# Performance work log

Hardware: AMD Instinct MI355X
Metric: run time of the kernel (lower is better)

The kernel has to match this reference:

```python
import jax, jax.numpy as jnp
import numpy as np

B, N, K, D, H, PQ, PV = 2, 2048, 30, 128, 4, 8, 4
INV3C = float(np.sqrt(1.0 / (3 * D)))      # 1/sqrt(3*hidden_dim)
INV3 = float(np.sqrt(1.0 / 3.0))
PT_SCALE = float(np.sqrt(1.0 / (3 * (PQ * 9.0 / 2))))


def _gather(nodes, idx):
    # nodes [B,N,...], idx [B,N,K] -> [B,N,K,...]
    return jax.vmap(lambda n, i: n[i])(nodes, idx)


def _ln(x, w, b, eps=1e-5):
    mu = x.mean(-1, keepdims=True)
    var = x.var(-1, keepdims=True)
    return (x - mu) / jnp.sqrt(var + eps) * w + b


def _forward(h_V, h_E, E_idx, R, t, mask_attend, mask_V,
             Wq, bq, Wkv, bkv, Wqp, bqp, Wkvp, bkvp, Wb, bb_, head_weights,
             Wout, bout, ln0_w, ln0_b, ln1_w, ln1_b, Wm1, bm1, Wm2, bm2):
    q = (h_V @ Wq + bq).reshape(B, N, H, D)                     # [B,N,H,C]
    kv = (h_V @ Wkv + bkv).reshape(B, N, H, 2 * D)
    k_, v_ = kv[..., :D], kv[..., D:]

    def apply_rigid(pts):  # pts [B,N,P,3] -> R @ p + t
        return jnp.einsum('bnxy,bnpy->bnpx', R, pts) + t[:, :, None, :]

    # torch builds points by split-into-3-then-stack along last dim
    qp = h_V @ Wqp + bqp                                        # [B,N,H*PQ*3]
    q_pts = jnp.stack(jnp.split(qp, 3, axis=-1), axis=-1)       # [B,N,H*PQ,3]
    q_pts = apply_rigid(q_pts).reshape(B, N, H, PQ, 3)
    kvp = h_V @ Wkvp + bkvp
    kv_pts = jnp.stack(jnp.split(kvp, 3, axis=-1), axis=-1)
    kv_pts = apply_rigid(kv_pts).reshape(B, N, H, PQ + PV, 3)
    k_pts, v_pts = kv_pts[..., :PQ, :], kv_pts[..., PQ:, :]

    b_bias = h_E @ Wb + bb_                                     # [B,N,K,H]
    k_nb = _gather(k_, E_idx)                                   # [B,N,K,H,C]
    a = jnp.einsum('bnhc,bnkhc->bnkh', q, k_nb) * INV3C
    a = a + INV3 * b_bias

    kp_nb = _gather(k_pts, E_idx)                               # [B,N,K,H,PQ,3]
    diff = q_pts[:, :, None] - kp_nb
    pt_att = jnp.sum(diff * diff, axis=-1)                      # [B,N,K,H,PQ]
    hw = jax.nn.softplus(head_weights)                          # [H]
    pt_att = jnp.sum(PT_SCALE * hw[None, None, None, :, None] * pt_att, axis=-1) * -0.5

    att_mask = 100000.0 * (mask_attend - 1.0)                   # [B,N,K]
    a = a + pt_att + att_mask[..., None]
    a = jax.nn.softmax(a, axis=-2)                              # softmax over neighbors K

    v_nb = _gather(v_, E_idx)
    o = jnp.einsum('bnkh,bnkhc->bnhc', a, v_nb).reshape(B, N, H * D)
    vp_nb = _gather(v_pts, E_idx)                               # [B,N,K,H,PV,3]
    o_pt = jnp.einsum('bnkh,bnkhpx->bnhpx', a, vp_nb)
    # invert_apply: R^T (x - t)
    o_pt = jnp.einsum('bnyx,bnhpy->bnhpx', R, o_pt - t[:, :, None, None, :])
    o_pt_norm = jnp.sqrt(jnp.sum(o_pt ** 2, axis=-1) + 1e-8).reshape(B, N, H * PV)
    o_pt = o_pt.reshape(B, N, H * PV, 3)
    o_pair = jnp.einsum('bnkh,bnkc->bnhc', a, h_E).reshape(B, N, H * D)

    cat = jnp.concatenate([o, o_pt[..., 0], o_pt[..., 1], o_pt[..., 2], o_pt_norm, o_pair], axis=-1)
    s = cat @ Wout + bout

    hv = _ln(h_V + s, ln0_w, ln0_b)
    m = jax.nn.relu(hv @ Wm1 + bm1) @ Wm2 + bm2
    hv = _ln(hv + m, ln1_w, ln1_b)
    return hv * mask_V[..., None]


def setup_inputs() -> dict:
    key = jax.random.key(0)
    ks = jax.random.split(key, 16)

    def dense(k, fi, fo):
        kw, kb = jax.random.split(k)
        s = 1.0 / np.sqrt(fi)
        return (jax.random.uniform(kw, (fi, fo), jnp.float32, -s, s),
                jax.random.uniform(kb, (fo,), jnp.float32, -s, s))

    h_V = jax.random.normal(ks[0], (B, N, D), jnp.float32)
    h_E = jax.random.normal(ks[1], (B, N, K, D), jnp.float32)
    E_idx = jax.random.randint(ks[2], (B, N, K), 0, N)
    Rr = jax.random.normal(ks[3], (B, N, 3, 3), jnp.float32)
    R, _ = jnp.linalg.qr(Rr)  # proper orthonormal frames
    t = jax.random.normal(ks[4], (B, N, 3), jnp.float32)
    mask_attend = jnp.ones((B, N, K), jnp.float32)
    mask_V = jnp.ones((B, N), jnp.float32)

    Wq, bq = dense(ks[5], D, D * H)
    Wkv, bkv = dense(ks[6], D, 2 * D * H)
    Wqp, bqp = dense(ks[7], D, H * PQ * 3)
    Wkvp, bkvp = dense(ks[8], D, H * (PQ + PV) * 3)
    Wb, bb_ = dense(ks[9], D, H)
    head_weights = jnp.full((H,), 0.541324854612918, jnp.float32)
    out_dim = H * (D + D + 4 * PV)
    Wout, bout = dense(ks[10], out_dim, D)
    ln0_w = jnp.ones((D,), jnp.float32); ln0_b = jnp.zeros((D,), jnp.float32)
    ln1_w = jnp.ones((D,), jnp.float32); ln1_b = jnp.zeros((D,), jnp.float32)
    Wm1, bm1 = dense(ks[11], D, 4 * D)
    Wm2, bm2 = dense(ks[12], 4 * D, D)
    return dict(h_V=h_V, h_E=h_E, E_idx=E_idx, R=R, t=t,
                mask_attend=mask_attend, mask_V=mask_V,
                Wq=Wq, bq=bq, Wkv=Wkv, bkv=bkv, Wqp=Wqp, bqp=bqp,
                Wkvp=Wkvp, bkvp=bkvp, Wb=Wb, bb_=bb_, head_weights=head_weights,
                Wout=Wout, bout=bout, ln0_w=ln0_w, ln0_b=ln0_b,
                ln1_w=ln1_w, ln1_b=ln1_b, Wm1=Wm1, bm1=bm1, Wm2=Wm2, bm2=bm2)


def reference(h_V, h_E, E_idx, R, t, mask_attend, mask_V,
              Wq, bq, Wkv, bkv, Wqp, bqp, Wkvp, bkvp, Wb, bb_, head_weights,
              Wout, bout, ln0_w, ln0_b, ln1_w, ln1_b, Wm1, bm1, Wm2, bm2):
    return _forward(h_V, h_E, E_idx, R, t, mask_attend, mask_V,
                    Wq, bq, Wkv, bkv, Wqp, bqp, Wkvp, bkvp, Wb, bb_, head_weights,
                    Wout, bout, ln0_w, ln0_b, ln1_w, ln1_b, Wm1, bm1, Wm2, bm2)
```

## Files before the change

kernel.cpp:

```cpp
#include <hip/hip_runtime.h>
#include <math.h>

#define BB 2
#define NN 2048
#define KK 30
#define DD 128
#define HH 4
#define PQ_ 8
#define PV_ 4
#define NPB 8
#define TM 16

#define INV3C    0.05103103630798288f
#define INV3     0.5773502691896258f
#define PT_SCALE 0.09622504486493764f

typedef __attribute__((ext_vector_type(8))) short short8;
typedef __attribute__((ext_vector_type(4))) float f32x4;
typedef __attribute__((ext_vector_type(4))) unsigned short us4;
typedef unsigned short ushort_t;

__device__ __forceinline__ ushort_t f2bf(float f) {
    unsigned u = __float_as_uint(f);
    unsigned r = u + 0x7FFFu + ((u >> 16) & 1u);
    return (ushort_t)(r >> 16);
}
__device__ __forceinline__ float bf2f(ushort_t u) {
    return __uint_as_float(((unsigned)u) << 16);
}

__device__ __forceinline__ void fma4(float4& a, float s, const float4& w) {
    a.x = fmaf(s, w.x, a.x);
    a.y = fmaf(s, w.y, a.y);
    a.z = fmaf(s, w.z, a.z);
    a.w = fmaf(s, w.w, a.w);
}

__global__ __launch_bounds__(256) void prep_kernel(
    const float* __restrict__ Wout, const float* __restrict__ Wm1,
    const float* __restrict__ Wm2,
    ushort_t* __restrict__ WoutT, ushort_t* __restrict__ Wm1T,
    ushort_t* __restrict__ Wm2T)
{
    const int stride = gridDim.x * blockDim.x;
    const int t0 = blockIdx.x * blockDim.x + threadIdx.x;
    for (int idx = t0; idx < 128 * 1088; idx += stride) {
        int n = idx / 1088, k = idx - n * 1088;
        WoutT[idx] = f2bf(Wout[(size_t)k * 128 + n]);
    }
    for (int idx = t0; idx < 512 * 128; idx += stride) {
        int n = idx >> 7, k = idx & 127;
        Wm1T[idx] = f2bf(Wm1[(size_t)k * 512 + n]);
    }
    for (int idx = t0; idx < 128 * 512; idx += stride) {
        int n = idx >> 9, k = idx & 511;
        Wm2T[idx] = f2bf(Wm2[(size_t)k * 128 + n]);
    }
}

__global__ __launch_bounds__(256, 4) void proj_kernel(
    const float* __restrict__ hV, const float* __restrict__ R, const float* __restrict__ tvec,
    const float* __restrict__ Wq, const float* __restrict__ bq,
    const float* __restrict__ Wkv, const float* __restrict__ bkv,
    const float* __restrict__ Wqp, const float* __restrict__ bqp,
    const float* __restrict__ Wkvp, const float* __restrict__ bkvp,
    float* __restrict__ q, ushort_t* __restrict__ kb, ushort_t* __restrict__ vb,
    float* __restrict__ qpts, float* __restrict__ kpts, float* __restrict__ vpts)
{
    const int node0 = (blockIdx.x >> 1) * NPB;
    const int half  = blockIdx.x & 1;
    const int tid = threadIdx.x;
    __shared__ float4 sx4[NPB][32];
    __shared__ float4 sqp4[NPB][24];
    __shared__ float4 skvp4[NPB][36];

    {
        const float4* src = (const float4*)(hV + (size_t)node0 * DD);
        sx4[tid >> 5][tid & 31] = src[tid];
    }
    __syncthreads();

    if (tid < 222) {
        const int Q = half * 222 + tid;
        const float* W; const float* bias; int ncols, col, dest;
        if (Q < 128)      { W = Wq;   bias = bq;   ncols = 512;  col = Q * 4;         dest = 0; }
        else if (Q < 384) { W = Wkv;  bias = bkv;  ncols = 1024; col = (Q - 128) * 4; dest = 1; }
        else if (Q < 408) { W = Wqp;  bias = bqp;  ncols = 96;   col = (Q - 384) * 4; dest = 2; }
        else              { W = Wkvp; bias = bkvp; ncols = 144;  col = (Q - 408) * 4; dest = 3; }

        float4 acc[NPB];
        #pragma unroll
        for (int r = 0; r < NPB; ++r) acc[r] = make_float4(0.f, 0.f, 0.f, 0.f);

        float4 w0 = *(const float4*)&W[(size_t)0 * ncols + col];
        float4 w1 = *(const float4*)&W[(size_t)1 * ncols + col];
        float4 w2 = *(const float4*)&W[(size_t)2 * ncols + col];
        float4 w3 = *(const float4*)&W[(size_t)3 * ncols + col];
        for (int i = 0; i < DD; i += 4) {
            float4 n0, n1, n2, n3;
            if (i + 4 < DD) {
                n0 = *(const float4*)&W[(size_t)(i + 4) * ncols + col];
                n1 = *(const float4*)&W[(size_t)(i + 5) * ncols + col];
                n2 = *(const float4*)&W[(size_t)(i + 6) * ncols + col];
                n3 = *(const float4*)&W[(size_t)(i + 7) * ncols + col];
            }
            #pragma unroll
            for (int r = 0; r < NPB; ++r) {
                float4 x = sx4[r][i >> 2];
                fma4(acc[r], x.x, w0);
                fma4(acc[r], x.y, w1);
                fma4(acc[r], x.z, w2);
                fma4(acc[r], x.w, w3);
            }
            w0 = n0; w1 = n1; w2 = n2; w3 = n3;
        }

        float4 bv = *(const float4*)&bias[col];
        if (dest == 0) {
            #pragma unroll
            for (int r = 0; r < NPB; ++r) {
                float4 o = make_float4(acc[r].x + bv.x, acc[r].y + bv.y,
                                       acc[r].z + bv.z, acc[r].w + bv.w);
                *(float4*)&q[(size_t)(node0 + r) * 512 + col] = o;
            }
        } else if (dest == 1) {
            int h = col >> 8, wcol = col & 255;
            ushort_t* base = (wcol < 128) ? kb : vb;
            int off = h * DD + (wcol & 127);
            #pragma unroll
            for (int r = 0; r < NPB; ++r) {
                us4 o;
                o.x = f2bf(acc[r].x + bv.x);
                o.y = f2bf(acc[r].y + bv.y);
                o.z = f2bf(acc[r].z + bv.z);
                o.w = f2bf(acc[r].w + bv.w);
                *(us4*)&base[(size_t)(node0 + r) * 512 + off] = o;
            }
        } else if (dest == 2) {
            #pragma unroll
            for (int r = 0; r < NPB; ++r) {
                float4 o = make_float4(acc[r].x + bv.x, acc[r].y + bv.y,
                                       acc[r].z + bv.z, acc[r].w + bv.w);
                sqp4[r][col >> 2] = o;
            }
        } else {
            #pragma unroll
            for (int r = 0; r < NPB; ++r) {
                float4 o = make_float4(acc[r].x + bv.x, acc[r].y + bv.y,
                                       acc[r].z + bv.z, acc[r].w + bv.w);
                skvp4[r][col >> 2] = o;
            }
        }
    }
    __syncthreads();

    if (half == 1) {
        const float* sqp_s  = (const float*)&sqp4[0][0];
        const float* skvp_s = (const float*)&skvp4[0][0];

        for (int idx = tid; idx < NPB * 96; idx += 256) {
            int r = idx / 96, u = idx % 96;
            int j = u / 3, d = u % 3;
            int node = node0 + r;
            float acc = tvec[node * 3 + d];
            #pragma unroll
            for (int y = 0; y < 3; ++y)
                acc = fmaf(R[node * 9 + d * 3 + y], sqp_s[r * 96 + y * 32 + j], acc);
            qpts[(size_t)node * 96 + j * 3 + d] = acc;
        }
        for (int idx = tid; idx < NPB * 144; idx += 256) {
            int r = idx / 144, u = idx % 144;
            int jj = u / 3, d = u % 3;
            int node = node0 + r;
            float acc = tvec[node * 3 + d];
            #pragma unroll
            for (int y = 0; y < 3; ++y)
                acc = fmaf(R[node * 9 + d * 3 + y], skvp_s[r * 144 + y * 48 + jj], acc);
            int hh = jj / 12, pp = jj % 12;
            if (pp < PQ_) kpts[(size_t)node * 96 + (hh * PQ_ + pp) * 3 + d] = acc;
            else          vpts[(size_t)node * 48 + (hh * PV_ + (pp - PQ_)) * 3 + d] = acc;
        }
    }
}

__global__ __launch_bounds__(256, 8) void attn_kernel(
    const float* __restrict__ hE, const int* __restrict__ Eidx,
    const float* __restrict__ R, const float* __restrict__ tvec,
    const float* __restrict__ mask_att,
    const float* __restrict__ Wb, const float* __restrict__ bb,
    const float* __restrict__ head_w,
    const float* __restrict__ q, const ushort_t* __restrict__ kb,
    const ushort_t* __restrict__ vb,
    const float* __restrict__ qpts, const float* __restrict__ kpts, const float* __restrict__ vpts,
    ushort_t* __restrict__ catb)
{
    const int node = blockIdx.x;
    const int b = node >> 11;
    const int tid = threadIdx.x;
    const int lane = tid & 63;
    const int wv = tid >> 6;

    __shared__ ushort_t s_hEb[KK * DD];
    __shared__ float s_cat[1088];
    __shared__ float s_qp[96];
    __shared__ float s_p[HH][32];
    __shared__ int   s_j[32];
    __shared__ float s_mask[32];
    __shared__ float s_opt[48];

    if (tid < 96) s_qp[tid] = qpts[(size_t)node * 96 + tid];
    if (tid < KK) {
        s_j[tid] = Eidx[(size_t)node * KK + tid];
        s_mask[tid] = 100000.0f * (mask_att[(size_t)node * KK + tid] - 1.0f);
    }
    __syncthreads();

    const int h = wv;
    const int l32 = lane & 31;
    const int g = lane >> 5;
    const float* hE_node = hE + (size_t)node * (KK * DD);

    const float q0  = q[(size_t)node * 512 + h * DD + l32];
    const float q1  = q[(size_t)node * 512 + h * DD + l32 + 32];
    const float q2  = q[(size_t)node * 512 + h * DD + l32 + 64];
    const float q3  = q[(size_t)node * 512 + h * DD + l32 + 96];
    const float wb0 = Wb[(l32 +  0) * HH + h];
    const float wb1 = Wb[(l32 + 32) * HH + h];
    const float wb2 = Wb[(l32 + 64) * HH + h];
    const float wb3 = Wb[(l32 + 96) * HH + h];
    const float cpt = -0.5f * PT_SCALE * log1pf(expf(head_w[h]));
    const float bbh = INV3 * bb[h];
    const float qpl = (l32 < 24) ? s_qp[h * 24 + l32] : 0.f;

    for (int kx2 = 0; kx2 < KK / 2; ++kx2) {
        const int k = kx2 * 2 + g;
        size_t jb = (size_t)(b * NN + s_j[k]);
        const ushort_t* kr = kb + jb * 512 + h * DD;
        float k0 = bf2f(kr[l32]),      k1 = bf2f(kr[l32 + 32]);
        float k2 = bf2f(kr[l32 + 64]), k3 = bf2f(kr[l32 + 96]);
        float s = q0 * k0 + q1 * k1 + q2 * k2 + q3 * k3;
        const float* her = hE_node + k * DD;
        float h0 = her[l32], h1 = her[l32 + 32], h2 = her[l32 + 64], h3 = her[l32 + 96];
        if (wv == 0) {
            s_hEb[k * DD + l32]      = f2bf(h0);
            s_hEb[k * DD + l32 + 32] = f2bf(h1);
            s_hEb[k * DD + l32 + 64] = f2bf(h2);
            s_hEb[k * DD + l32 + 96] = f2bf(h3);
        }
        float t = wb0 * h0 + wb1 * h1 + wb2 * h2 + wb3 * h3;
        float ptc = 0.f;
        if (l32 < 24) {
            float d = qpl - kpts[jb * 96 + h * 24 + l32];
            ptc = d * d;
        }
        float val = INV3C * s + INV3 * t + cpt * ptc;
        #pragma unroll
        for (int off = 16; off; off >>= 1) val += __shfl_down(val, off, 32);
        if (l32 == 0) s_p[h][k] = val + bbh + s_mask[k];
    }
    __syncthreads();

    {
        float v = (lane < KK) ? s_p[h][lane] : -INFINITY;
        float m = v;
        #pragma unroll
        for (int off = 16; off; off >>= 1) m = fmaxf(m, __shfl_down(m, off));
        m = __shfl(m, 0);
        float e = (lane < KK) ? expf(v - m) : 0.f;
        float s = e;
        #pragma unroll
        for (int off = 16; off; off >>= 1) s += __shfl_down(s, off);
        s = __shfl(s, 0);
        if (lane < KK) s_p[h][lane] = e / s;
    }
    __syncthreads();

    {
        const int oh = tid >> 6;
        const int oc0 = (tid & 63) * 2;
        float a0 = 0.f, a1 = 0.f;
        for (int kx = 0; kx < KK; ++kx) {
            size_t jb = (size_t)(b * NN + s_j[kx]);
            unsigned pv = *(const unsigned*)&vb[jb * 512 + oh * DD + oc0];
            float p = s_p[oh][kx];
            a0 = fmaf(p, bf2f((ushort_t)(pv & 0xffff)), a0);
            a1 = fmaf(p, bf2f((ushort_t)(pv >> 16)), a1);
        }
        s_cat[oh * DD + oc0]     = a0;
        s_cat[oh * DD + oc0 + 1] = a1;
        float b0 = 0.f, b1 = 0.f;
        for (int kx = 0; kx < KK; ++kx) {
            unsigned pe = *(const unsigned*)&s_hEb[kx * DD + oc0];
            float p = s_p[oh][kx];
            b0 = fmaf(p, bf2f((ushort_t)(pe & 0xffff)), b0);
            b1 = fmaf(p, bf2f((ushort_t)(pe >> 16)), b1);
        }
        s_cat[576 + oh * DD + oc0]     = b0;
        s_cat[576 + oh * DD + oc0 + 1] = b1;
    }
    if (tid < 48) {
        int jj = tid / 3, d = tid % 3;
        int oh = jj >> 2;
        float acc = 0.f;
        for (int kx = 0; kx < KK; ++kx) {
            size_t jb = (size_t)(b * NN + s_j[kx]);
            acc = fmaf(s_p[oh][kx], vpts[jb * 48 + jj * 3 + d], acc);
        }
        s_opt[tid] = acc;
    }
    __syncthreads();
    if (tid < 16) {
        int jj = tid;
        float g0 = s_opt[jj * 3 + 0] - tvec[node * 3 + 0];
        float g1 = s_opt[jj * 3 + 1] - tvec[node * 3 + 1];
        float g2 = s_opt[jj * 3 + 2] - tvec[node * 3 + 2];
        float l0 = R[node * 9 + 0] * g0 + R[node * 9 + 3] * g1 + R[node * 9 + 6] * g2;
        float l1 = R[node * 9 + 1] * g0 + R[node * 9 + 4] * g1 + R[node * 9 + 7] * g2;
        float l2 = R[node * 9 + 2] * g0 + R[node * 9 + 5] * g1 + R[node * 9 + 8] * g2;
        s_cat[512 + 0 * 16 + jj] = l0;
        s_cat[512 + 1 * 16 + jj] = l1;
        s_cat[512 + 2 * 16 + jj] = l2;
        s_cat[560 + jj] = sqrtf(l0 * l0 + l1 * l1 + l2 * l2 + 1e-8f);
    }
    __syncthreads();

    for (int i = tid; i < 1088; i += 256)
        catb[(size_t)node * 1088 + i] = f2bf(s_cat[i]);
}

__global__ __launch_bounds__(512) void tail_kernel(
    const float* __restrict__ hV, const float* __restrict__ maskV,
    const ushort_t* __restrict__ catb,
    const ushort_t* __restrict__ WoutT, const float* __restrict__ bout,
    const float* __restrict__ ln0w, const float* __restrict__ ln0b,
    const float* __restrict__ ln1w, const float* __restrict__ ln1b,
    const ushort_t* __restrict__ Wm1T, const float* __restrict__ bm1,
    const ushort_t* __restrict__ Wm2T, const float* __restrict__ bm2,
    float* __restrict__ out)
{
    const int node0 = blockIdx.x * TM;
    const int tid = threadIdx.x;
    const int w  = tid >> 6;
    const int l  = tid & 63;
    const int lr = l & 15;
    const int lk = l >> 4;

    __shared__ float    s_x[TM][DD];
    __shared__ float    s_hv[TM][DD];
    __shared__ ushort_t s_hvb[TM][136];
    __shared__ ushort_t s_m1[TM][520];
    __shared__ float    s_rs[TM][16];
    __shared__ float    s_rq[TM][16];
    __shared__ float    s_stat[TM][2];

    {
        f32x4 acc = {0.f, 0.f, 0.f, 0.f};
        const ushort_t* Ab = catb + (size_t)(node0 + lr) * 1088 + lk * 8;
        const ushort_t* Bb = WoutT + (size_t)(w * 16 + lr) * 1088 + lk * 8;
        #pragma unroll 2
        for (int ks = 0; ks < 34; ++ks) {
            short8 a = *(const short8*)(Ab + ks * 32);
            short8 bfr = *(const short8*)(Bb + ks * 32);
            acc = __builtin_amdgcn_mfma_f32_16x16x32_bf16(a, bfr, acc, 0, 0, 0);
        }
        #pragma unroll
        for (int i = 0; i < 4; ++i)
            s_x[lk * 4 + i][w * 16 + lr] = acc[i];
    }
    __syncthreads();

    if (tid < 256) {
        int r = tid >> 4, sg = tid & 15;
        float ss = 0.f, sq = 0.f;
        #pragma unroll
        for (int j = 0; j < 8; ++j) {
            int cc = sg * 8 + j;
            float x = s_x[r][cc] + bout[cc] + hV[(size_t)(node0 + r) * DD + cc];
            s_x[r][cc] = x;
            ss += x; sq += x * x;
        }
        s_rs[r][sg] = ss; s_rq[r][sg] = sq;
    }
    __syncthreads();
    if (tid < TM) {
        float ss = 0.f, sq = 0.f;
        #pragma unroll
        for (int sg = 0; sg < 16; ++sg) { ss += s_rs[tid][sg]; sq += s_rq[tid][sg]; }
        float mu = ss / 128.f;
        s_stat[tid][0] = mu;
        s_stat[tid][1] = rsqrtf(sq / 128.f - mu * mu + 1e-5f);
    }
    __syncthreads();
    {
        int idx = tid * 4;
        int r = idx >> 7, cc = idx & 127;
        float mu = s_stat[r][0], rstd = s_stat[r][1];
        #pragma unroll
        for (int j = 0; j < 4; ++j) {
            float hvv = (s_x[r][cc + j] - mu) * rstd * ln0w[cc + j] + ln0b[cc + j];
            s_hv[r][cc + j] = hvv;
            s_hvb[r][cc + j] = f2bf(hvv);
        }
    }
    __syncthreads();

    {
        const ushort_t* Ab = &s_hvb[lr][lk * 8];
        #pragma unroll
        for (int t = 0; t < 4; ++t) {
            int n0 = w * 64 + t * 16;
            f32x4 acc = {0.f, 0.f, 0.f, 0.f};
            const ushort_t* Bb = Wm1T + (size_t)(n0 + lr) * 128 + lk * 8;
            #pragma unroll
            for (int ks = 0; ks < 4; ++ks) {
                short8 a = *(const short8*)(Ab + ks * 32);
                short8 bfr = *(const short8*)(Bb + ks * 32);
                acc = __builtin_amdgcn_mfma_f32_16x16x32_bf16(a, bfr, acc, 0, 0, 0);
            }
            int n = n0 + lr;
            float bm = bm1[n];
            #pragma unroll
            for (int i = 0; i < 4; ++i)
                s_m1[lk * 4 + i][n] = f2bf(fmaxf(acc[i] + bm, 0.f));
        }
    }
    __syncthreads();

    {
        f32x4 acc = {0.f, 0.f, 0.f, 0.f};
        const ushort_t* Ab = &s_m1[lr][lk * 8];
        const ushort_t* Bb = Wm2T + (size_t)(w * 16 + lr) * 512 + lk * 8;
        #pragma unroll 4
        for (int ks = 0; ks < 16; ++ks) {
            short8 a = *(const short8*)(Ab + ks * 32);
            short8 bfr = *(const short8*)(Bb + ks * 32);
            acc = __builtin_amdgcn_mfma_f32_16x16x32_bf16(a, bfr, acc, 0, 0, 0);
        }
        #pragma unroll
        for (int i = 0; i < 4; ++i)
            s_x[lk * 4 + i][w * 16 + lr] = acc[i];
    }
    __syncthreads();

    if (tid < 256) {
        int r = tid >> 4, sg = tid & 15;
        float ss = 0.f, sq = 0.f;
        #pragma unroll
        for (int j = 0; j < 8; ++j) {
            int cc = sg * 8 + j;
            float x = s_x[r][cc] + bm2[cc] + s_hv[r][cc];
            s_x[r][cc] = x;
            ss += x; sq += x * x;
        }
        s_rs[r][sg] = ss; s_rq[r][sg] = sq;
    }
    __syncthreads();
    if (tid < TM) {
        float ss = 0.f, sq = 0.f;
        #pragma unroll
        for (int sg = 0; sg < 16; ++sg) { ss += s_rs[tid][sg]; sq += s_rq[tid][sg]; }
        float mu = ss / 128.f;
        s_stat[tid][0] = mu;
        s_stat[tid][1] = rsqrtf(sq / 128.f - mu * mu + 1e-5f);
    }
    __syncthreads();
    {
        int idx = tid * 4;
        int r = idx >> 7, cc = idx & 127;
        float mu = s_stat[r][0], rstd = s_stat[r][1];
        float mk = maskV[node0 + r];
        float4 o;
        o.x = ((s_x[r][cc + 0] - mu) * rstd * ln1w[cc + 0] + ln1b[cc + 0]) * mk;
        o.y = ((s_x[r][cc + 1] - mu) * rstd * ln1w[cc + 1] + ln1b[cc + 1]) * mk;
        o.z = ((s_x[r][cc + 2] - mu) * rstd * ln1w[cc + 2] + ln1b[cc + 2]) * mk;
        o.w = ((s_x[r][cc + 3] - mu) * rstd * ln1w[cc + 3] + ln1b[cc + 3]) * mk;
        *(float4*)&out[(size_t)(node0 + r) * DD + cc] = o;
    }
}

extern "C" void kernel_launch(void* const* d_in, const int* in_sizes, int n_in,
                              void* d_out, int out_size, void* d_ws, size_t ws_size,
                              hipStream_t stream)
{
    const float* hV      = (const float*)d_in[0];
    const float* hE      = (const float*)d_in[1];
    const int*   Eidx    = (const int*)  d_in[2];
    const float* R       = (const float*)d_in[3];
    const float* tvec    = (const float*)d_in[4];
    const float* mask_at = (const float*)d_in[5];
    const float* maskV   = (const float*)d_in[6];
    const float* Wq      = (const float*)d_in[7];
    const float* bq      = (const float*)d_in[8];
    const float* Wkv     = (const float*)d_in[9];
    const float* bkv     = (const float*)d_in[10];
    const float* Wqp     = (const float*)d_in[11];
    const float* bqp     = (const float*)d_in[12];
    const float* Wkvp    = (const float*)d_in[13];
    const float* bkvp    = (const float*)d_in[14];
    const float* Wb      = (const float*)d_in[15];
    const float* bb      = (const float*)d_in[16];
    const float* hw      = (const float*)d_in[17];
    const float* Wout    = (const float*)d_in[18];
    const float* bout    = (const float*)d_in[19];
    const float* ln0w    = (const float*)d_in[20];
    const float* ln0b    = (const float*)d_in[21];
    const float* ln1w    = (const float*)d_in[22];
    const float* ln1b    = (const float*)d_in[23];
    const float* Wm1     = (const float*)d_in[24];
    const float* bm1     = (const float*)d_in[25];
    const float* Wm2     = (const float*)d_in[26];
    const float* bm2     = (const float*)d_in[27];

    const size_t nodes = (size_t)BB * NN;
    float* ws  = (float*)d_ws;
    float* q   = ws;
    float* qp  = q  + nodes * 512;
    float* kp  = qp + nodes * 96;
    float* vp  = kp + nodes * 96;
    ushort_t* kb    = (ushort_t*)(vp + nodes * 48);
    ushort_t* vb    = kb + nodes * 512;
    ushort_t* catb  = vb + nodes * 512;
    ushort_t* WoutT = catb  + nodes * 1088;
    ushort_t* Wm1T  = WoutT + 128 * 1088;
    ushort_t* Wm2T  = Wm1T  + 512 * 128;

    prep_kernel<<<256, 256, 0, stream>>>(Wout, Wm1, Wm2, WoutT, Wm1T, Wm2T);

    proj_kernel<<<(int)(nodes / NPB) * 2, 256, 0, stream>>>(
        hV, R, tvec, Wq, bq, Wkv, bkv, Wqp, bqp, Wkvp, bkvp,
        q, kb, vb, qp, kp, vp);

    attn_kernel<<<(int)nodes, 256, 0, stream>>>(
        hE, Eidx, R, tvec, mask_at,
        Wb, bb, hw,
        q, kb, vb, qp, kp, vp, catb);

    tail_kernel<<<(int)(nodes / TM), 512, 0, stream>>>(
        hV, maskV, catb,
        WoutT, bout, ln0w, ln0b, ln1w, ln1b,
        Wm1T, bm1, Wm2T, bm2, (float*)d_out);
}
```

Baseline: 119.0 us.

## Move projection GEMM to bf16 MFMA, store q in bf16, prefetch value gathers

The projection kernel now runs on bf16 MFMA 16x16x32 instructions instead of scalar FP32 FMAs. Its weights are packed into one transposed bf16 matrix in the prep kernel, with 16 nodes per block and 512 threads. The query is stored as bf16 and loaded as packed pairs, and the key loads in attention become 32-bit packed reads. The value and point gathers in attention are software-prefetched in groups of six neighbors. This cuts FP32 ALU work and memory traffic, at the cost of lower precision for q and the point projections.

```diff
diff --git a/kernel.cpp b/kernel.cpp
--- a/kernel.cpp
+++ b/kernel.cpp
@@ -8,7 +8,6 @@
 #define HH 4
 #define PQ_ 8
 #define PV_ 4
-#define NPB 8
 #define TM 16
 
 #define INV3C    0.05103103630798288f
@@ -17,7 +16,6 @@
 
 typedef __attribute__((ext_vector_type(8))) short short8;
 typedef __attribute__((ext_vector_type(4))) float f32x4;
-typedef __attribute__((ext_vector_type(4))) unsigned short us4;
 typedef unsigned short ushort_t;
 
 __device__ __forceinline__ ushort_t f2bf(float f) {
@@ -28,19 +26,20 @@
 __device__ __forceinline__ float bf2f(ushort_t u) {
     return __uint_as_float(((unsigned)u) << 16);
 }
-
-__device__ __forceinline__ void fma4(float4& a, float s, const float4& w) {
-    a.x = fmaf(s, w.x, a.x);
-    a.y = fmaf(s, w.y, a.y);
-    a.z = fmaf(s, w.z, a.z);
-    a.w = fmaf(s, w.w, a.w);
+__device__ __forceinline__ float bflo(unsigned u) {
+    return __uint_as_float(u << 16);
+}
+__device__ __forceinline__ float bfhi(unsigned u) {
+    return __uint_as_float(u & 0xffff0000u);
 }
 
 __global__ __launch_bounds__(256) void prep_kernel(
     const float* __restrict__ Wout, const float* __restrict__ Wm1,
     const float* __restrict__ Wm2,
+    const float* __restrict__ Wq, const float* __restrict__ Wkv,
+    const float* __restrict__ Wqp, const float* __restrict__ Wkvp,
     ushort_t* __restrict__ WoutT, ushort_t* __restrict__ Wm1T,
-    ushort_t* __restrict__ Wm2T)
+    ushort_t* __restrict__ Wm2T, ushort_t* __restrict__ WprojT)
 {
     const int stride = gridDim.x * blockDim.x;
     const int t0 = blockIdx.x * blockDim.x + threadIdx.x;
@@ -56,126 +55,102 @@
         int n = idx >> 9, k = idx & 511;
         Wm2T[idx] = f2bf(Wm2[(size_t)k * 128 + n]);
     }
-}
-
-__global__ __launch_bounds__(256, 4) void proj_kernel(
+    for (int idx = t0; idx < 1792 * 128; idx += stride) {
+        int n = idx >> 7, k = idx & 127;
+        float v;
+        if (n < 512)       v = Wq[(size_t)k * 512 + n];
+        else if (n < 1536) v = Wkv[(size_t)k * 1024 + (n - 512)];
+        else if (n < 1632) v = Wqp[k * 96 + (n - 1536)];
+        else if (n < 1776) v = Wkvp[k * 144 + (n - 1632)];
+        else               v = 0.f;
+        WprojT[idx] = f2bf(v);
+    }
+}
+
+__global__ __launch_bounds__(512) void proj_kernel(
     const float* __restrict__ hV, const float* __restrict__ R, const float* __restrict__ tvec,
-    const float* __restrict__ Wq, const float* __restrict__ bq,
-    const float* __restrict__ Wkv, const float* __restrict__ bkv,
-    const float* __restrict__ Wqp, const float* __restrict__ bqp,
-    const float* __restrict__ Wkvp, const float* __restrict__ bkvp,
-    float* __restrict__ q, ushort_t* __restrict__ kb, ushort_t* __restrict__ vb,
+    const ushort_t* __restrict__ WT,
+    const float* __restrict__ bq, const float* __restrict__ bkv,
+    const float* __restrict__ bqp, const float* __restrict__ bkvp,
+    ushort_t* __restrict__ qb, ushort_t* __restrict__ kb, ushort_t* __restrict__ vb,
     float* __restrict__ qpts, float* __restrict__ kpts, float* __restrict__ vpts)
 {
-    const int node0 = (blockIdx.x >> 1) * NPB;
+    const int node0 = (blockIdx.x >> 1) * TM;
     const int half  = blockIdx.x & 1;
     const int tid = threadIdx.x;
-    __shared__ float4 sx4[NPB][32];
-    __shared__ float4 sqp4[NPB][24];
-    __shared__ float4 skvp4[NPB][36];
-
-    {
-        const float4* src = (const float4*)(hV + (size_t)node0 * DD);
-        sx4[tid >> 5][tid & 31] = src[tid];
-    }
-    __syncthreads();
-
-    if (tid < 222) {
-        const int Q = half * 222 + tid;
-        const float* W; const float* bias; int ncols, col, dest;
-        if (Q < 128)      { W = Wq;   bias = bq;   ncols = 512;  col = Q * 4;         dest = 0; }
-        else if (Q < 384) { W = Wkv;  bias = bkv;  ncols = 1024; col = (Q - 128) * 4; dest = 1; }
-        else if (Q < 408) { W = Wqp;  bias = bqp;  ncols = 96;   col = (Q - 384) * 4; dest = 2; }
-        else              { W = Wkvp; bias = bkvp; ncols = 144;  col = (Q - 408) * 4; dest = 3; }
-
-        float4 acc[NPB];
-        #pragma unroll
-        for (int r = 0; r < NPB; ++r) acc[r] = make_float4(0.f, 0.f, 0.f, 0.f);
-
-        float4 w0 = *(const float4*)&W[(size_t)0 * ncols + col];
-        float4 w1 = *(const float4*)&W[(size_t)1 * ncols + col];
-        float4 w2 = *(const float4*)&W[(size_t)2 * ncols + col];
-        float4 w3 = *(const float4*)&W[(size_t)3 * ncols + col];
-        for (int i = 0; i < DD; i += 4) {
-            float4 n0, n1, n2, n3;
-            if (i + 4 < DD) {
-                n0 = *(const float4*)&W[(size_t)(i + 4) * ncols + col];
-                n1 = *(const float4*)&W[(size_t)(i + 5) * ncols + col];
-                n2 = *(const float4*)&W[(size_t)(i + 6) * ncols + col];
-                n3 = *(const float4*)&W[(size_t)(i + 7) * ncols + col];
-            }
-            #pragma unroll
-            for (int r = 0; r < NPB; ++r) {
-                float4 x = sx4[r][i >> 2];
-                fma4(acc[r], x.x, w0);
-                fma4(acc[r], x.y, w1);
-                fma4(acc[r], x.z, w2);
-                fma4(acc[r], x.w, w3);
-            }
-            w0 = n0; w1 = n1; w2 = n2; w3 = n3;
-        }
-
-        float4 bv = *(const float4*)&bias[col];
-        if (dest == 0) {
-            #pragma unroll
-            for (int r = 0; r < NPB; ++r) {
-                float4 o = make_float4(acc[r].x + bv.x, acc[r].y + bv.y,
-                                       acc[r].z + bv.z, acc[r].w + bv.w);
-                *(float4*)&q[(size_t)(node0 + r) * 512 + col] = o;
-            }
-        } else if (dest == 1) {
-            int h = col >> 8, wcol = col & 255;
+    const int w = tid >> 6, l = tid & 63, lr = l & 15, lk = l >> 4;
+
+    __shared__ ushort_t s_A[TM][128];
+    __shared__ float s_qp[TM][96];
+    __shared__ float s_kvp[TM][144];
+
+    {
+        int i = tid * 4; int r = i >> 7, c = i & 127;
+        float4 x = *(const float4*)&hV[(size_t)(node0 + r) * DD + c];
+        s_A[r][c + 0] = f2bf(x.x); s_A[r][c + 1] = f2bf(x.y);
+        s_A[r][c + 2] = f2bf(x.z); s_A[r][c + 3] = f2bf(x.w);
+    }
+    __syncthreads();
+
+    const ushort_t* Ab = &s_A[lr][lk * 8];
+    for (int t = 0; t < 7; ++t) {
+        const int tile = half * 56 + w * 7 + t;
+        const int n = tile * 16 + lr;
+        f32x4 acc = {0.f, 0.f, 0.f, 0.f};
+        const ushort_t* Bb = WT + (size_t)n * 128 + lk * 8;
+        #pragma unroll
+        for (int ks = 0; ks < 4; ++ks) {
+            short8 a = *(const short8*)(Ab + ks * 32);
+            short8 bfr = *(const short8*)(Bb + ks * 32);
+            acc = __builtin_amdgcn_mfma_f32_16x16x32_bf16(a, bfr, acc, 0, 0, 0);
+        }
+        if (n < 512) {
+            float bias = bq[n];
+            #pragma unroll
+            for (int i = 0; i < 4; ++i)
+                qb[(size_t)(node0 + lk * 4 + i) * 512 + n] = f2bf(acc[i] + bias);
+        } else if (n < 1536) {
+            int n2 = n - 512;
+            float bias = bkv[n2];
+            int hh = n2 >> 8, wcol = n2 & 255;
             ushort_t* base = (wcol < 128) ? kb : vb;
-            int off = h * DD + (wcol & 127);
-            #pragma unroll
-            for (int r = 0; r < NPB; ++r) {
-                us4 o;
-                o.x = f2bf(acc[r].x + bv.x);
-                o.y = f2bf(acc[r].y + bv.y);
-                o.z = f2bf(acc[r].z + bv.z);
-                o.w = f2bf(acc[r].w + bv.w);
-                *(us4*)&base[(size_t)(node0 + r) * 512 + off] = o;
-            }
-        } else if (dest == 2) {
-            #pragma unroll
-            for (int r = 0; r < NPB; ++r) {
-                float4 o = make_float4(acc[r].x + bv.x, acc[r].y + bv.y,
-                                       acc[r].z + bv.z, acc[r].w + bv.w);
-                sqp4[r][col >> 2] = o;
-            }
-        } else {
-            #pragma unroll
-            for (int r = 0; r < NPB; ++r) {
-                float4 o = make_float4(acc[r].x + bv.x, acc[r].y + bv.y,
-                                       acc[r].z + bv.z, acc[r].w + bv.w);
-                skvp4[r][col >> 2] = o;
-            }
+            int off = hh * DD + (wcol & 127);
+            #pragma unroll
+            for (int i = 0; i < 4; ++i)
+                base[(size_t)(node0 + lk * 4 + i) * 512 + off] = f2bf(acc[i] + bias);
+        } else if (n < 1632) {
+            int c = n - 1536;
+            float bias = bqp[c];
+            #pragma unroll
+            for (int i = 0; i < 4; ++i) s_qp[lk * 4 + i][c] = acc[i] + bias;
+        } else if (n < 1776) {
+            int c = n - 1632;
+            float bias = bkvp[c];
+            #pragma unroll
+            for (int i = 0; i < 4; ++i) s_kvp[lk * 4 + i][c] = acc[i] + bias;
         }
     }
     __syncthreads();
 
     if (half == 1) {
-        const float* sqp_s  = (const float*)&sqp4[0][0];
-        const float* skvp_s = (const float*)&skvp4[0][0];
-
-        for (int idx = tid; idx < NPB * 96; idx += 256) {
+        for (int idx = tid; idx < TM * 96; idx += 512) {
             int r = idx / 96, u = idx % 96;
             int j = u / 3, d = u % 3;
             int node = node0 + r;
             float acc = tvec[node * 3 + d];
             #pragma unroll
             for (int y = 0; y < 3; ++y)
-                acc = fmaf(R[node * 9 + d * 3 + y], sqp_s[r * 96 + y * 32 + j], acc);
+                acc = fmaf(R[node * 9 + d * 3 + y], s_qp[r][y * 32 + j], acc);
             qpts[(size_t)node * 96 + j * 3 + d] = acc;
         }
-        for (int idx = tid; idx < NPB * 144; idx += 256) {
+        for (int idx = tid; idx < TM * 144; idx += 512) {
             int r = idx / 144, u = idx % 144;
             int jj = u / 3, d = u % 3;
             int node = node0 + r;
             float acc = tvec[node * 3 + d];
             #pragma unroll
             for (int y = 0; y < 3; ++y)
-                acc = fmaf(R[node * 9 + d * 3 + y], skvp_s[r * 144 + y * 48 + jj], acc);
+                acc = fmaf(R[node * 9 + d * 3 + y], s_kvp[r][y * 48 + jj], acc);
             int hh = jj / 12, pp = jj % 12;
             if (pp < PQ_) kpts[(size_t)node * 96 + (hh * PQ_ + pp) * 3 + d] = acc;
             else          vpts[(size_t)node * 48 + (hh * PV_ + (pp - PQ_)) * 3 + d] = acc;
@@ -189,7 +164,7 @@
     const float* __restrict__ mask_att,
     const float* __restrict__ Wb, const float* __restrict__ bb,
     const float* __restrict__ head_w,
-    const float* __restrict__ q, const ushort_t* __restrict__ kb,
+    const ushort_t* __restrict__ qb, const ushort_t* __restrict__ kb,
     const ushort_t* __restrict__ vb,
     const float* __restrict__ qpts, const float* __restrict__ kpts, const float* __restrict__ vpts,
     ushort_t* __restrict__ catb)
@@ -220,10 +195,9 @@
     const int g = lane >> 5;
     const float* hE_node = hE + (size_t)node * (KK * DD);
 
-    const float q0  = q[(size_t)node * 512 + h * DD + l32];
-    const float q1  = q[(size_t)node * 512 + h * DD + l32 + 32];
-    const float q2  = q[(size_t)node * 512 + h * DD + l32 + 64];
-    const float q3  = q[(size_t)node * 512 + h * DD + l32 + 96];
+    const unsigned qu0 = *(const unsigned*)&qb[(size_t)node * 512 + h * DD + 2 * l32];
+    const unsigned qu1 = *(const unsigned*)&qb[(size_t)node * 512 + h * DD + 64 + 2 * l32];
+    const float q0 = bflo(qu0), q1 = bfhi(qu0), q2 = bflo(qu1), q3 = bfhi(qu1);
     const float wb0 = Wb[(l32 +  0) * HH + h];
     const float wb1 = Wb[(l32 + 32) * HH + h];
     const float wb2 = Wb[(l32 + 64) * HH + h];
@@ -236,9 +210,9 @@
         const int k = kx2 * 2 + g;
         size_t jb = (size_t)(b * NN + s_j[k]);
         const ushort_t* kr = kb + jb * 512 + h * DD;
-        float k0 = bf2f(kr[l32]),      k1 = bf2f(kr[l32 + 32]);
-        float k2 = bf2f(kr[l32 + 64]), k3 = bf2f(kr[l32 + 96]);
-        float s = q0 * k0 + q1 * k1 + q2 * k2 + q3 * k3;
+        unsigned ku0 = *(const unsigned*)&kr[2 * l32];
+        unsigned ku1 = *(const unsigned*)&kr[64 + 2 * l32];
+        float s = q0 * bflo(ku0) + q1 * bfhi(ku0) + q2 * bflo(ku1) + q3 * bfhi(ku1);
         const float* her = hE_node + k * DD;
         float h0 = her[l32], h1 = her[l32 + 32], h2 = her[l32 + 64], h3 = her[l32 + 96];
         if (wv == 0) {
@@ -278,33 +252,58 @@
     {
         const int oh = tid >> 6;
         const int oc0 = (tid & 63) * 2;
-        float a0 = 0.f, a1 = 0.f;
-        for (int kx = 0; kx < KK; ++kx) {
-            size_t jb = (size_t)(b * NN + s_j[kx]);
-            unsigned pv = *(const unsigned*)&vb[jb * 512 + oh * DD + oc0];
-            float p = s_p[oh][kx];
-            a0 = fmaf(p, bf2f((ushort_t)(pv & 0xffff)), a0);
-            a1 = fmaf(p, bf2f((ushort_t)(pv >> 16)), a1);
-        }
-        s_cat[oh * DD + oc0]     = a0;
-        s_cat[oh * DD + oc0 + 1] = a1;
-        float b0 = 0.f, b1 = 0.f;
-        for (int kx = 0; kx < KK; ++kx) {
-            unsigned pe = *(const unsigned*)&s_hEb[kx * DD + oc0];
-            float p = s_p[oh][kx];
-            b0 = fmaf(p, bf2f((ushort_t)(pe & 0xffff)), b0);
-            b1 = fmaf(p, bf2f((ushort_t)(pe >> 16)), b1);
-        }
+        const ushort_t* vrow = vb + oh * DD + oc0;
+        float a0 = 0.f, a1 = 0.f, b0 = 0.f, b1 = 0.f;
+        unsigned buf[6];
+        #pragma unroll
+        for (int j = 0; j < 6; ++j)
+            buf[j] = *(const unsigned*)(vrow + (size_t)(b * NN + s_j[j]) * 512);
+        #pragma unroll
+        for (int base = 0; base < KK; base += 6) {
+            unsigned nbuf[6];
+            if (base + 6 < KK) {
+                #pragma unroll
+                for (int j = 0; j < 6; ++j)
+                    nbuf[j] = *(const unsigned*)(vrow + (size_t)(b * NN + s_j[base + 6 + j]) * 512);
+            }
+            #pragma unroll
+            for (int j = 0; j < 6; ++j) {
+                const int kx = base + j;
+                float p = s_p[oh][kx];
+                a0 = fmaf(p, bflo(buf[j]), a0);
+                a1 = fmaf(p, bfhi(buf[j]), a1);
+                unsigned pe = *(const unsigned*)&s_hEb[kx * DD + oc0];
+                b0 = fmaf(p, bflo(pe), b0);
+                b1 = fmaf(p, bfhi(pe), b1);
+            }
+            #pragma unroll
+            for (int j = 0; j < 6; ++j) buf[j] = nbuf[j];
+        }
+        s_cat[oh * DD + oc0]           = a0;
+        s_cat[oh * DD + oc0 + 1]       = a1;
         s_cat[576 + oh * DD + oc0]     = b0;
         s_cat[576 + oh * DD + oc0 + 1] = b1;
     }
     if (tid < 48) {
-        int jj = tid / 3, d = tid % 3;
-        int oh = jj >> 2;
+        const int oh = (tid / 3) >> 2;
         float acc = 0.f;
-        for (int kx = 0; kx < KK; ++kx) {
-            size_t jb = (size_t)(b * NN + s_j[kx]);
-            acc = fmaf(s_p[oh][kx], vpts[jb * 48 + jj * 3 + d], acc);
+        float fb[6];
+        #pragma unroll
+        for (int j = 0; j < 6; ++j)
+            fb[j] = vpts[(size_t)(b * NN + s_j[j]) * 48 + tid];
+        #pragma unroll
+        for (int base = 0; base < KK; base += 6) {
+            float nb[6];
+            if (base + 6 < KK) {
+                #pragma unroll
+                for (int j = 0; j < 6; ++j)
+                    nb[j] = vpts[(size_t)(b * NN + s_j[base + 6 + j]) * 48 + tid];
+            }
+            #pragma unroll
+            for (int j = 0; j < 6; ++j)
+                acc = fmaf(s_p[oh][base + j], fb[j], acc);
+            #pragma unroll
+            for (int j = 0; j < 6; ++j) fb[j] = nb[j];
         }
         s_opt[tid] = acc;
     }
@@ -512,28 +511,29 @@
     const float* bm2     = (const float*)d_in[27];
 
     const size_t nodes = (size_t)BB * NN;
-    float* ws  = (float*)d_ws;
-    float* q   = ws;
-    float* qp  = q  + nodes * 512;
-    float* kp  = qp + nodes * 96;
-    float* vp  = kp + nodes * 96;
-    ushort_t* kb    = (ushort_t*)(vp + nodes * 48);
-    ushort_t* vb    = kb + nodes * 512;
-    ushort_t* catb  = vb + nodes * 512;
-    ushort_t* WoutT = catb  + nodes * 1088;
-    ushort_t* Wm1T  = WoutT + 128 * 1088;
-    ushort_t* Wm2T  = Wm1T  + 512 * 128;
-
-    prep_kernel<<<256, 256, 0, stream>>>(Wout, Wm1, Wm2, WoutT, Wm1T, Wm2T);
-
-    proj_kernel<<<(int)(nodes / NPB) * 2, 256, 0, stream>>>(
-        hV, R, tvec, Wq, bq, Wkv, bkv, Wqp, bqp, Wkvp, bkvp,
-        q, kb, vb, qp, kp, vp);
+    ushort_t* qb     = (ushort_t*)d_ws;
+    ushort_t* kb     = qb + nodes * 512;
+    ushort_t* vb     = kb + nodes * 512;
+    ushort_t* catb   = vb + nodes * 512;
+    ushort_t* WoutT  = catb + nodes * 1088;
+    ushort_t* Wm1T   = WoutT + 128 * 1088;
+    ushort_t* Wm2T   = Wm1T + 512 * 128;
+    ushort_t* WprojT = Wm2T + 128 * 512;
+    float* qpts = (float*)(WprojT + 1792 * 128);
+    float* kpts = qpts + nodes * 96;
+    float* vpts = kpts + nodes * 96;
+
+    prep_kernel<<<256, 256, 0, stream>>>(Wout, Wm1, Wm2, Wq, Wkv, Wqp, Wkvp,
+                                         WoutT, Wm1T, Wm2T, WprojT);
+
+    proj_kernel<<<(int)(nodes / TM) * 2, 512, 0, stream>>>(
+        hV, R, tvec, WprojT, bq, bkv, bqp, bkvp,
+        qb, kb, vb, qpts, kpts, vpts);
 
     attn_kernel<<<(int)nodes, 256, 0, stream>>>(
         hE, Eidx, R, tvec, mask_at,
         Wb, bb, hw,
-        q, kb, vb, qp, kp, vp, catb);
+        qb, kb, vb, qpts, kpts, vpts, catb);
 
     tail_kernel<<<(int)(nodes / TM), 512, 0, stream>>>(
         hV, maskV, catb,
```

Result: no change. 117.4 us (-1.4%).
